# Kernel optimization log

Measured on AMD Instinct MI355X. Metric: run time of the kernel, lower is better.

## Reference

```python
import jax, jax.numpy as jnp
import numpy as np

TEMP = 0.1
K = 4
EPS = 1e-12


def _normalize(x):
    return x / jnp.maximum(jnp.linalg.norm(x, axis=1, keepdims=True), 1e-12)


def _sq_dists(a, b):
    # a: [Na,3], b: [Nb,3] -> [Na,Nb] squared euclidean distances
    aa = jnp.sum(a * a, axis=1, keepdims=True)          # [Na,1]
    bb = jnp.sum(b * b, axis=1, keepdims=True).T        # [1,Nb]
    return aa + bb - 2.0 * (a @ b.T)


def _directional_loss(f_q, f_db, d2_q_db):
    # knn of each query point in the database cloud, then cosine-sim softmax self-consistency loss
    _, idx = jax.lax.top_k(-d2_q_db, K)                  # [Nq,K] nearest-db indices
    f_matched = f_db[idx]                                # [Nq,K,C] gather (pointops.grouping)
    sim = jnp.einsum('nc,nkc->nk', f_q, f_matched) / TEMP
    p = jax.nn.softmax(sim, axis=1)                      # q_i == softmax when use_sinkhorn=False
    return jnp.mean(-jnp.log(jnp.sum(p * p, axis=1) + EPS))


def setup_inputs() -> dict:
    key = jax.random.key(0)
    k1, k2, k3, k4 = jax.random.split(key, 4)
    return {
        'feat_i': jax.random.normal(k1, (20000, 96), dtype=jnp.float32),
        'coord_i': jax.random.uniform(k2, (20000, 3), dtype=jnp.float32),
        'feat_j': jax.random.normal(k3, (10000, 96), dtype=jnp.float32),
        'coord_j': jax.random.uniform(k4, (10000, 3), dtype=jnp.float32),
    }


def reference(feat_i, coord_i, feat_j, coord_j):
    fi = _normalize(feat_i)
    fj = _normalize(feat_j)
    d2 = _sq_dists(coord_i, coord_j)                     # [Ni,Nj]
    loss_i = _directional_loss(fi, fj, d2)               # i queries, j database
    loss_j = _directional_loss(fj, fi, d2.T)             # j queries, i database
    pair = (loss_i + loss_j) * 0.5
    # num_views = 2 -> total_loss / max(1, num_views - 1) = pair
    return pair
```

## Files before the change

### kernel.cpp

```cpp
#include <hip/hip_runtime.h>
#include <math.h>

#define KMASK 0xFFFF8000u
#define IMASK 0x7FFFu

__device__ __forceinline__ float wave_reduce_sum(float v) {
    #pragma unroll
    for (int off = 32; off >= 1; off >>= 1) v += __shfl_xor(v, off, 64);
    return v;
}

__device__ __forceinline__ unsigned wave_min_u32(unsigned v) {
    #pragma unroll
    for (int off = 32; off >= 1; off >>= 1) {
        unsigned o = (unsigned)__shfl_xor((int)v, off, 64);
        v = (o < v) ? o : v;
    }
    return v;
}

__device__ __forceinline__ unsigned gmin8(unsigned v) {
    #pragma unroll
    for (int off = 4; off >= 1; off >>= 1) {
        unsigned o = (unsigned)__shfl_xor((int)v, off, 64);
        v = (o < v) ? o : v;
    }
    return v;
}
__device__ __forceinline__ float gsum8(float v) {
    #pragma unroll
    for (int off = 4; off >= 1; off >>= 1) v += __shfl_xor(v, off, 64);
    return v;
}

__device__ __forceinline__ void insert4kv(unsigned k, unsigned v,
                                          unsigned (&bk)[4], unsigned (&bv)[4]) {
    const bool c0 = k < bk[0], c1 = k < bk[1], c2 = k < bk[2], c3 = k < bk[3];
    bk[3] = c2 ? bk[2] : (c3 ? k : bk[3]);
    bv[3] = c2 ? bv[2] : (c3 ? v : bv[3]);
    bk[2] = c1 ? bk[1] : (c2 ? k : bk[2]);
    bv[2] = c1 ? bv[1] : (c2 ? v : bv[2]);
    bk[1] = c0 ? bk[0] : (c1 ? k : bk[1]);
    bv[1] = c0 ? bv[0] : (c1 ? v : bv[1]);
    bk[0] = c0 ? k : bk[0];
    bv[0] = c0 ? v : bv[0];
}

__device__ __forceinline__ int cell_of(float x, int G) {
    int c = (int)(x * (float)G);
    return (c < 0) ? 0 : ((c >= G) ? G - 1 : c);
}

__device__ __forceinline__ float dot4(float4 a, float4 b) {
    return fmaf(a.w, b.w, fmaf(a.z, b.z, fmaf(a.y, b.y, a.x * b.x)));
}


__global__ __launch_bounds__(256)
void grid_zero(int* __restrict__ stA, int nA, int* __restrict__ stB, int nB,
               float* __restrict__ out)
{
    const int t = blockIdx.x * 256 + threadIdx.x;
    if (t < nA) stA[t] = 0;
    if (t < nB) stB[t] = 0;
    if (t == 0) out[0] = 0.0f;
}

__global__ __launch_bounds__(256)
void grid_count(const float* __restrict__ cA, int nA, int GA, int* __restrict__ stA,
                const float* __restrict__ cB, int nB, int GB, int* __restrict__ stB)
{
    const int t = blockIdx.x * 256 + threadIdx.x;
    const float* c; int* s; int G; int p;
    if (t < nA)           { c = cA; s = stA; G = GA; p = t; }
    else if (t < nA + nB) { c = cB; s = stB; G = GB; p = t - nA; }
    else return;
    const int cx = cell_of(c[3*p], G), cy = cell_of(c[3*p+1], G), cz = cell_of(c[3*p+2], G);
    atomicAdd(&s[(cz * G + cy) * G + cx + 1], 1);
}

__global__ __launch_bounds__(256)
void grid_scan(int* __restrict__ sA, int nA, int* __restrict__ cuA,
               int* __restrict__ sB, int nB, int* __restrict__ cuB)
{
    int* s  = blockIdx.x ? sB  : sA;
    int* cu = blockIdx.x ? cuB : cuA;
    const int n = blockIdx.x ? nB : nA;
    __shared__ int part[256];
    const int t = threadIdx.x;
    const int len = n + 1;
    const int chunk = (len + 255) >> 8;
    const int lo = t * chunk;
    const int hi = (lo + chunk < len) ? (lo + chunk) : len;
    int sum = 0;
    for (int i = lo; i < hi; ++i) sum += s[i];
    part[t] = sum;
    __syncthreads();
    for (int d = 1; d < 256; d <<= 1) {
        const int v = (t >= d) ? part[t - d] : 0;
        __syncthreads();
        part[t] += v;
        __syncthreads();
    }
    int run = (t > 0) ? part[t - 1] : 0;
    for (int i = lo; i < hi; ++i) {
        run += s[i];
        s[i] = run;
        if (i < n) cu[i] = run;
    }
}

__global__ __launch_bounds__(256)
void grid_scatter(const float* __restrict__ cA, int nA, int GA, int* __restrict__ cuA,
                  float4* __restrict__ soA,
                  const float* __restrict__ cB, int nB, int GB, int* __restrict__ cuB,
                  float4* __restrict__ soB)
{
    const int t = blockIdx.x * 256 + threadIdx.x;
    const float* c; int* cu; float4* so; int G; int p;
    if (t < nA)           { c = cA; cu = cuA; so = soA; G = GA; p = t; }
    else if (t < nA + nB) { c = cB; cu = cuB; so = soB; G = GB; p = t - nA; }
    else return;
    const float x = c[3*p], y = c[3*p+1], z = c[3*p+2];
    const int cx = cell_of(x, G), cy = cell_of(y, G), cz = cell_of(z, G);
    const int pos = atomicAdd(&cu[(cz * G + cy) * G + cx], 1);
    so[pos] = make_float4(x, y, z, __uint_as_float((unsigned)p));
}


__global__ __launch_bounds__(256)
void knnloss(const float* __restrict__ fi, int Ni,
             const float* __restrict__ fj, int Nj,
             const float4* __restrict__ soA, const int* __restrict__ stA, int GA,
             const float4* __restrict__ soB, const int* __restrict__ stB, int GB,
             float sc0, float sc1, float* __restrict__ out)
{
    const int sub = threadIdx.x & 7;
    const int qid = (blockIdx.x * 256 + threadIdx.x) >> 3;
    float acc = 0.0f;

    if (qid < Ni + Nj) {
        const bool d0 = (qid < Ni);
        const int sq = d0 ? qid : qid - Ni;
        const float4* soq = d0 ? soB : soA;
        const float4* so = d0 ? soA : soB;
        const int*    st = d0 ? stA : stB;
        const int      G = d0 ? GA  : GB;
        const int     nd = d0 ? Nj  : Ni;
        const float*  fd = d0 ? fj  : fi;
        const float scale = d0 ? sc0 : sc1;

        const float4 Q = soq[sq];
        const unsigned p = __float_as_uint(Q.w);
        const float* fqp = (d0 ? fi : fj) + (size_t)p * 96;

        const float4* q4 = (const float4*)fqp;
        const float4 qa = q4[3*sub], qb = q4[3*sub+1], qc = q4[3*sub+2];

        const float qx = Q.x, qy = Q.y, qz = Q.z;
        const float h = 1.0f / (float)G;
        const int cx = cell_of(qx, G), cy = cell_of(qy, G), cz = cell_of(qz, G);
        unsigned nk[4], nv[4];

        {
            const int x0 = max(cx - 1, 0), x1 = min(cx + 1, G - 1);
            int csr[9], cer[9];
            #pragma unroll
            for (int dz = 0; dz < 3; ++dz) {
                #pragma unroll
                for (int dy = 0; dy < 3; ++dy) {
                    const int zz = cz + dz - 1, yy = cy + dy - 1;
                    const bool v = ((unsigned)zz < (unsigned)G) & ((unsigned)yy < (unsigned)G);
                    const int rb = v ? (zz * G + yy) * G : 0;
                    csr[dz*3+dy] = v ? st[rb + x0] : 0;
                    cer[dz*3+dy] = v ? st[rb + x1 + 1] : 0;
                }
            }
            unsigned bk[4] = {~0u, ~0u, ~0u, ~0u};
            unsigned bv[4] = {~0u, ~0u, ~0u, ~0u};
            #pragma unroll
            for (int r = 0; r < 9; ++r) {
                const int ce = cer[r];
                for (int cc = csr[r] + sub; cc < ce; cc += 16) {
                    const float4 P0 = so[cc];
                    const int cc1 = cc + 8;
                    const bool v1 = (cc1 < ce);
                    float4 P1 = P0;
                    if (v1) P1 = so[cc1];
                    const float dx0 = P0.x - qx, dy0 = P0.y - qy, dz0 = P0.z - qz;
                    const float d20 = fmaf(dx0, dx0, fmaf(dy0, dy0, dz0 * dz0));
                    const unsigned k0 = (__float_as_uint(d20) & KMASK) | (unsigned)cc;
                    insert4kv(k0, __float_as_uint(P0.w), bk, bv);
                    const float dx1 = P1.x - qx, dy1 = P1.y - qy, dz1 = P1.z - qz;
                    const float d21 = fmaf(dx1, dx1, fmaf(dy1, dy1, dz1 * dz1));
                    unsigned k1 = (__float_as_uint(d21) & KMASK) | (unsigned)cc1;
                    if (!v1) k1 = ~0u;
                    insert4kv(k1, __float_as_uint(P1.w), bk, bv);
                }
            }
            unsigned k0 = bk[0], k1 = bk[1], k2 = bk[2], k3 = bk[3];
            unsigned v0 = bv[0], v1 = bv[1], v2 = bv[2], v3 = bv[3];
            #pragma unroll
            for (int r = 0; r < 4; ++r) {
                const unsigned m = gmin8(k0);
                const bool win = (k0 == m);
                nv[r] = gmin8(win ? v0 : ~0u);
                nk[r] = m;
                k0 = win ? k1 : k0; v0 = win ? v1 : v0;
                k1 = win ? k2 : k1; v1 = win ? v2 : v1;
                k2 = win ? k3 : k2; v2 = win ? v3 : v2;
                k3 = win ? ~0u : k3;
            }
            const int y0 = max(cy - 1, 0), y1 = min(cy + 1, G - 1);
            const int z0 = max(cz - 1, 0), z1 = min(cz + 1, G - 1);
            float margin = 3.0e38f;
            if (x0 > 0)     margin = fminf(margin, qx - (float)x0 * h);
            if (x1 < G - 1) margin = fminf(margin, (float)(x1 + 1) * h - qx);
            if (y0 > 0)     margin = fminf(margin, qy - (float)y0 * h);
            if (y1 < G - 1) margin = fminf(margin, (float)(y1 + 1) * h - qy);
            if (z0 > 0)     margin = fminf(margin, qz - (float)z0 * h);
            if (z1 < G - 1) margin = fminf(margin, (float)(z1 + 1) * h - qz);
            const bool covered = (margin > 1.0e37f);
            const float kd = __uint_as_float(nk[3] & KMASK);
            const bool ok = covered || (kd * 1.01f <= margin * margin);

            if (!ok) {
                for (int s = 2; ; ++s) {
                    const int sx0 = max(cx - s, 0), sx1 = min(cx + s, G - 1);
                    const int sy0 = max(cy - s, 0), sy1 = min(cy + s, G - 1);
                    const int sz0 = max(cz - s, 0), sz1 = min(cz + s, G - 1);
                    unsigned b2k[4] = {~0u, ~0u, ~0u, ~0u};
                    unsigned b2v[4] = {~0u, ~0u, ~0u, ~0u};
                    for (int z = sz0; z <= sz1; ++z) {
                        for (int y = sy0; y <= sy1; ++y) {
                            const int rb = (z * G + y) * G;
                            const int cs = st[rb + sx0];
                            const int ce = st[rb + sx1 + 1];
                            for (int cc = cs + sub; cc < ce; cc += 8) {
                                const float4 P = so[cc];
                                const float dx = P.x - qx, dy = P.y - qy, dz = P.z - qz;
                                const float d2 = fmaf(dx, dx, fmaf(dy, dy, dz * dz));
                                const unsigned k =
                                    (__float_as_uint(d2) & KMASK) | (unsigned)cc;
                                insert4kv(k, __float_as_uint(P.w), b2k, b2v);
                            }
                        }
                    }
                    unsigned u0 = b2k[0], u1 = b2k[1], u2 = b2k[2], u3 = b2k[3];
                    unsigned w0 = b2v[0], w1 = b2v[1], w2 = b2v[2], w3 = b2v[3];
                    #pragma unroll
                    for (int r = 0; r < 4; ++r) {
                        const unsigned m = gmin8(u0);
                        const bool win = (u0 == m);
                        nv[r] = gmin8(win ? w0 : ~0u);
                        nk[r] = m;
                        u0 = win ? u1 : u0; w0 = win ? w1 : w0;
                        u1 = win ? u2 : u1; w1 = win ? w2 : w1;
                        u2 = win ? u3 : u2; w2 = win ? w3 : w2;
                        u3 = win ? ~0u : u3;
                    }
                    float mg = 3.0e38f;
                    if (sx0 > 0)     mg = fminf(mg, qx - (float)sx0 * h);
                    if (sx1 < G - 1) mg = fminf(mg, (float)(sx1 + 1) * h - qx);
                    if (sy0 > 0)     mg = fminf(mg, qy - (float)sy0 * h);
                    if (sy1 < G - 1) mg = fminf(mg, (float)(sy1 + 1) * h - qy);
                    if (sz0 > 0)     mg = fminf(mg, qz - (float)sz0 * h);
                    if (sz1 < G - 1) mg = fminf(mg, (float)(sz1 + 1) * h - qz);
                    const bool cov = (mg > 1.0e37f);
                    const float k2d = __uint_as_float(nk[3] & KMASK);
                    if (cov || (k2d * 1.01f <= mg * mg)) break;
                }
            }
        }

        const unsigned nm1 = (unsigned)(nd - 1);
        const unsigned i0 = nv[0] < nm1 ? nv[0] : nm1;
        const unsigned i1 = nv[1] < nm1 ? nv[1] : nm1;
        const unsigned i2 = nv[2] < nm1 ? nv[2] : nm1;
        const unsigned i3 = nv[3] < nm1 ? nv[3] : nm1;

        const float4* f0 = (const float4*)(fd + (size_t)i0 * 96);
        const float4* f1 = (const float4*)(fd + (size_t)i1 * 96);
        const float4* f2 = (const float4*)(fd + (size_t)i2 * 96);
        const float4* f3 = (const float4*)(fd + (size_t)i3 * 96);
        const float4 a0 = f0[3*sub], b0 = f0[3*sub+1], c0 = f0[3*sub+2];
        const float4 a1 = f1[3*sub], b1 = f1[3*sub+1], c1 = f1[3*sub+2];
        const float4 a2 = f2[3*sub], b2 = f2[3*sub+1], c2 = f2[3*sub+2];
        const float4 a3 = f3[3*sub], b3 = f3[3*sub+1], c3 = f3[3*sub+2];

        const float ssq = gsum8(dot4(qa,qa) + dot4(qb,qb) + dot4(qc,qc));

        float sim[4];
        {
            const float dv = gsum8(dot4(qa,a0) + dot4(qb,b0) + dot4(qc,c0));
            const float sd = gsum8(dot4(a0,a0) + dot4(b0,b0) + dot4(c0,c0));
            sim[0] = dv * rsqrtf(fmaxf(ssq, 1e-24f) * fmaxf(sd, 1e-24f)) * 10.0f;
        }
        {
            const float dv = gsum8(dot4(qa,a1) + dot4(qb,b1) + dot4(qc,c1));
            const float sd = gsum8(dot4(a1,a1) + dot4(b1,b1) + dot4(c1,c1));
            sim[1] = dv * rsqrtf(fmaxf(ssq, 1e-24f) * fmaxf(sd, 1e-24f)) * 10.0f;
        }
        {
            const float dv = gsum8(dot4(qa,a2) + dot4(qb,b2) + dot4(qc,c2));
            const float sd = gsum8(dot4(a2,a2) + dot4(b2,b2) + dot4(c2,c2));
            sim[2] = dv * rsqrtf(fmaxf(ssq, 1e-24f) * fmaxf(sd, 1e-24f)) * 10.0f;
        }
        {
            const float dv = gsum8(dot4(qa,a3) + dot4(qb,b3) + dot4(qc,c3));
            const float sd = gsum8(dot4(a3,a3) + dot4(b3,b3) + dot4(c3,c3));
            sim[3] = dv * rsqrtf(fmaxf(ssq, 1e-24f) * fmaxf(sd, 1e-24f)) * 10.0f;
        }

        const float m = fmaxf(fmaxf(sim[0], sim[1]), fmaxf(sim[2], sim[3]));
        const float e0 = __expf(sim[0] - m), e1 = __expf(sim[1] - m);
        const float e2 = __expf(sim[2] - m), e3 = __expf(sim[3] - m);
        const float ssum = e0 + e1 + e2 + e3;
        const float inv = 1.0f / ssum;
        const float p2 = (e0*e0 + e1*e1 + e2*e2 + e3*e3) * inv * inv;
        if (sub == 0) acc = -__logf(p2 + 1e-12f) * scale;
    }

    acc = wave_reduce_sum(acc);
    __shared__ float red[4];
    if ((threadIdx.x & 63) == 0) red[threadIdx.x >> 6] = acc;
    __syncthreads();
    if (threadIdx.x == 0) atomicAdd(out, red[0] + red[1] + red[2] + red[3]);
}


#define WPB 4
__device__ __forceinline__ void insert4u(unsigned k, unsigned (&b)[4]) {
    const bool c0 = k < b[0], c1 = k < b[1], c2 = k < b[2], c3 = k < b[3];
    b[3] = c2 ? b[2] : (c3 ? k : b[3]);
    b[2] = c1 ? b[1] : (c2 ? k : b[2]);
    b[1] = c0 ? b[0] : (c1 ? k : b[1]);
    b[0] = c0 ? k : b[0];
}

template<int QPW>
__device__ __forceinline__ void brute_dir(
    const float* __restrict__ cq, const float* __restrict__ fq, int Nq,
    const float* __restrict__ cd, const float* __restrict__ fd, int Nd,
    float scale, float* __restrict__ out, int blk)
{
    const int lane = threadIdx.x & 63;
    const int widx = threadIdx.x >> 6;
    int qbase = (blk * WPB + widx) * QPW;
    if (qbase >= Nq) return;
    qbase = __builtin_amdgcn_readfirstlane(qbase);

    float qx[QPW], qy[QPW], qz[QPW];
    #pragma unroll
    for (int q = 0; q < QPW; ++q) {
        const int qi = (qbase + q < Nq) ? (qbase + q) : (Nq - 1);
        qx[q] = cq[qi*3]; qy[q] = cq[qi*3+1]; qz[q] = cq[qi*3+2];
    }
    unsigned bk[QPW][4];
    #pragma unroll
    for (int q = 0; q < QPW; ++q) {
        #pragma unroll
        for (int k = 0; k < 4; ++k) bk[q][k] = ~0u;
    }
    for (int base = 0; base < Nd; base += 64) {
        const int p = base + lane;
        const int cp = (p < Nd) ? p : (Nd - 1);
        const float px = cd[cp*3], py = cd[cp*3+1], pz = cd[cp*3+2];
        #pragma unroll
        for (int q = 0; q < QPW; ++q) {
            const float dx = px - qx[q], dy = py - qy[q], dz = pz - qz[q];
            const float d2 = dx*dx + dy*dy + dz*dz;
            unsigned k = (__float_as_uint(d2) & KMASK) | (unsigned)p;
            if (p >= Nd) k = ~0u;
            insert4u(k, bk[q]);
        }
    }
    float wacc = 0.0f;
    #pragma unroll
    for (int q = 0; q < QPW; ++q) {
        if (qbase + q >= Nq) break;
        unsigned t0 = bk[q][0], t1 = bk[q][1], t2 = bk[q][2], t3 = bk[q][3];
        int ni_[4];
        #pragma unroll
        for (int k = 0; k < 4; ++k) {
            const unsigned m = wave_min_u32(t0);
            ni_[k] = (int)(m & IMASK);
            const bool win = (t0 == m);
            t0 = win ? t1 : t0; t1 = win ? t2 : t1; t2 = win ? t3 : t2; t3 = win ? ~0u : t3;
        }
        const float* fqp = fq + (size_t)(qbase + q) * 96;
        const float qf0 = fqp[lane];
        const float qf1 = (lane < 32) ? fqp[64 + lane] : 0.0f;
        const float ssq = wave_reduce_sum(qf0*qf0 + qf1*qf1);
        float sim[4];
        #pragma unroll
        for (int k = 0; k < 4; ++k) {
            const float* fdp = fd + (size_t)ni_[k] * 96;
            const float df0 = fdp[lane];
            const float df1 = (lane < 32) ? fdp[64 + lane] : 0.0f;
            const float dotv = wave_reduce_sum(qf0*df0 + qf1*df1);
            const float ssd = wave_reduce_sum(df0*df0 + df1*df1);
            sim[k] = dotv * rsqrtf(fmaxf(ssq, 1e-24f) * fmaxf(ssd, 1e-24f)) * 10.0f;
        }
        const float m = fmaxf(fmaxf(sim[0], sim[1]), fmaxf(sim[2], sim[3]));
        const float e0 = __expf(sim[0]-m), e1 = __expf(sim[1]-m);
        const float e2 = __expf(sim[2]-m), e3 = __expf(sim[3]-m);
        const float ssum = e0+e1+e2+e3;
        const float inv = 1.0f/ssum;
        const float p2 = (e0*e0+e1*e1+e2*e2+e3*e3)*inv*inv;
        wacc += -__logf(p2 + 1e-12f);
    }
    if (lane == 0) atomicAdd(out, wacc * scale);
}

__global__ __launch_bounds__(256)
void brute_fused(const float* __restrict__ ci, const float* __restrict__ fi, int Ni,
                 const float* __restrict__ cj, const float* __restrict__ fj, int Nj,
                 float s0, float s1, int B0, int B1, float* __restrict__ out)
{
    const int bid = (int)blockIdx.x;
    const int bmin = (B0 < B1) ? B0 : B1;
    int dir, blk;
    if (bid < 2 * bmin) { dir = bid & 1; blk = bid >> 1; }
    else { dir = (B0 > B1) ? 0 : 1; blk = bid - bmin; }
    if (dir == 0) brute_dir<8>(ci, fi, Ni, cj, fj, Nj, s0, out, blk);
    else          brute_dir<4>(cj, fj, Nj, ci, fi, Ni, s1, out, blk);
}


extern "C" void kernel_launch(void* const* d_in, const int* in_sizes, int n_in,
                              void* d_out, int out_size, void* d_ws, size_t ws_size,
                              hipStream_t stream) {
    const float* feat_i  = (const float*)d_in[0];
    const float* coord_i = (const float*)d_in[1];
    const float* feat_j  = (const float*)d_in[2];
    const float* coord_j = (const float*)d_in[3];
    const int Ni = in_sizes[0] / 96;
    const int Nj = in_sizes[2] / 96;
    float* out = (float*)d_out;

    auto gridfor = [](int n) {
        int g = (int)cbrtf((float)n / 4.5f);
        if (g < 2) g = 2;
        if (g > 28) g = 28;
        return g;
    };
    const int GA = gridfor(Nj), GB = gridfor(Ni);
    const int GA3 = GA * GA * GA, GB3 = GB * GB * GB;

    size_t off = 0;
    auto alloc = [&](size_t bytes) { size_t o = off; off = (off + bytes + 15) & ~(size_t)15; return o; };
    const size_t o_soA  = alloc((size_t)Nj * 16);
    const size_t o_soB  = alloc((size_t)Ni * 16);
    const size_t o_stA  = alloc((size_t)(GA3 + 1) * 4);
    const size_t o_stB  = alloc((size_t)(GB3 + 1) * 4);
    const size_t o_cuA  = alloc((size_t)GA3 * 4);
    const size_t o_cuB  = alloc((size_t)GB3 * 4);

    if (ws_size >= off && Ni >= 16 && Nj >= 16 && Ni <= 32000 && Nj <= 32000) {
        char* W = (char*)d_ws;
        float4* soA = (float4*)(W + o_soA);
        float4* soB = (float4*)(W + o_soB);
        int* stA = (int*)(W + o_stA);
        int* stB = (int*)(W + o_stB);
        int* cuA = (int*)(W + o_cuA);
        int* cuB = (int*)(W + o_cuB);

        const int nPts = Ni + Nj;
        const int nmax = ((GA3 > GB3) ? GA3 : GB3) + 1;

        grid_zero<<<(nmax + 255) / 256, 256, 0, stream>>>(stA, GA3 + 1, stB, GB3 + 1, out);
        grid_count<<<(nPts + 255) / 256, 256, 0, stream>>>(
            coord_j, Nj, GA, stA, coord_i, Ni, GB, stB);
        grid_scan<<<2, 256, 0, stream>>>(stA, GA3, cuA, stB, GB3, cuB);
        grid_scatter<<<(nPts + 255) / 256, 256, 0, stream>>>(
            coord_j, Nj, GA, cuA, soA, coord_i, Ni, GB, cuB, soB);

        const int nQ = Ni + Nj;
        const int nblk = (nQ * 8 + 255) / 256;
        knnloss<<<nblk, 256, 0, stream>>>(
            feat_i, Ni, feat_j, Nj,
            soA, stA, GA, soB, stB, GB,
            0.5f / (float)Ni, 0.5f / (float)Nj, out);
    } else {
        hipMemsetAsync(out, 0, sizeof(float), stream);
        const int waves0 = (Ni + 7) / 8;
        const int B0 = (waves0 + WPB - 1) / WPB;
        const int waves1 = (Nj + 3) / 4;
        const int B1 = (waves1 + WPB - 1) / WPB;
        brute_fused<<<B0 + B1, 256, 0, stream>>>(
            coord_i, feat_i, Ni, coord_j, feat_j, Nj,
            0.5f / (float)Ni, 0.5f / (float)Nj, B0, B1, out);
    }
}
```

Baseline: 49.56 us.

## Fuse grid build and kNN loss into one cooperative kernel with grid syncs

Replaces the five separate launches (zero, count, scan, scatter, knnloss) with a single cooperative kernel that runs the same stages separated by grid-wide syncs. The kNN query body moves into a shared device function used by both the fused and the fallback paths. The aim is to remove per-launch overhead and the idle gaps between small kernels. In exchange it pays for four grid.sync barriers, leaves most blocks idle while two blocks do the scan, and the fused kernel's register use may lower occupancy. It also adds an occupancy query and a device attribute query on the host each call, and falls back to the old launches if the grid cannot be fully resident.

```diff
diff --git a/kernel.cpp b/kernel.cpp
--- a/kernel.cpp
+++ b/kernel.cpp
@@ -1,5 +1,8 @@
 #include <hip/hip_runtime.h>
+#include <hip/hip_cooperative_groups.h>
 #include <math.h>
+
+namespace cg = cooperative_groups;
 
 #define KMASK 0xFFFF8000u
 #define IMASK 0x7FFFu
@@ -53,6 +56,282 @@
 
 __device__ __forceinline__ float dot4(float4 a, float4 b) {
     return fmaf(a.w, b.w, fmaf(a.z, b.z, fmaf(a.y, b.y, a.x * b.x)));
+}
+
+__device__ __forceinline__ float knn_query(
+    int qid, int Ni, int Nj,
+    const float* __restrict__ fi, const float* __restrict__ fj,
+    const float4* __restrict__ soA, const int* __restrict__ stA, int GA,
+    const float4* __restrict__ soB, const int* __restrict__ stB, int GB,
+    float sc0, float sc1, int sub)
+{
+    const bool d0 = (qid < Ni);
+    const int sq = d0 ? qid : qid - Ni;
+    const float4* soq = d0 ? soB : soA;
+    const float4* so = d0 ? soA : soB;
+    const int*    st = d0 ? stA : stB;
+    const int      G = d0 ? GA  : GB;
+    const int     nd = d0 ? Nj  : Ni;
+    const float*  fd = d0 ? fj  : fi;
+    const float scale = d0 ? sc0 : sc1;
+
+    const float4 Q = soq[sq];
+    const unsigned p = __float_as_uint(Q.w);
+    const float* fqp = (d0 ? fi : fj) + (size_t)p * 96;
+
+    const float4* q4 = (const float4*)fqp;
+    const float4 qa = q4[3*sub], qb = q4[3*sub+1], qc = q4[3*sub+2];
+
+    const float qx = Q.x, qy = Q.y, qz = Q.z;
+    const float h = 1.0f / (float)G;
+    const int cx = cell_of(qx, G), cy = cell_of(qy, G), cz = cell_of(qz, G);
+    unsigned nk[4], nv[4];
+
+    {
+        const int x0 = max(cx - 1, 0), x1 = min(cx + 1, G - 1);
+        int csr[9], cer[9];
+        #pragma unroll
+        for (int dz = 0; dz < 3; ++dz) {
+            #pragma unroll
+            for (int dy = 0; dy < 3; ++dy) {
+                const int zz = cz + dz - 1, yy = cy + dy - 1;
+                const bool v = ((unsigned)zz < (unsigned)G) & ((unsigned)yy < (unsigned)G);
+                const int rb = v ? (zz * G + yy) * G : 0;
+                csr[dz*3+dy] = v ? st[rb + x0] : 0;
+                cer[dz*3+dy] = v ? st[rb + x1 + 1] : 0;
+            }
+        }
+        unsigned bk[4] = {~0u, ~0u, ~0u, ~0u};
+        unsigned bv[4] = {~0u, ~0u, ~0u, ~0u};
+        #pragma unroll
+        for (int r = 0; r < 9; ++r) {
+            const int ce = cer[r];
+            for (int cc = csr[r] + sub; cc < ce; cc += 16) {
+                const float4 P0 = so[cc];
+                const int cc1 = cc + 8;
+                const bool v1 = (cc1 < ce);
+                float4 P1 = P0;
+                if (v1) P1 = so[cc1];
+                const float dx0 = P0.x - qx, dy0 = P0.y - qy, dz0 = P0.z - qz;
+                const float d20 = fmaf(dx0, dx0, fmaf(dy0, dy0, dz0 * dz0));
+                const unsigned k0 = (__float_as_uint(d20) & KMASK) | (unsigned)cc;
+                insert4kv(k0, __float_as_uint(P0.w), bk, bv);
+                const float dx1 = P1.x - qx, dy1 = P1.y - qy, dz1 = P1.z - qz;
+                const float d21 = fmaf(dx1, dx1, fmaf(dy1, dy1, dz1 * dz1));
+                unsigned k1 = (__float_as_uint(d21) & KMASK) | (unsigned)cc1;
+                if (!v1) k1 = ~0u;
+                insert4kv(k1, __float_as_uint(P1.w), bk, bv);
+            }
+        }
+        unsigned k0 = bk[0], k1 = bk[1], k2 = bk[2], k3 = bk[3];
+        unsigned v0 = bv[0], v1 = bv[1], v2 = bv[2], v3 = bv[3];
+        #pragma unroll
+        for (int r = 0; r < 4; ++r) {
+            const unsigned m = gmin8(k0);
+            const bool win = (k0 == m);
+            nv[r] = gmin8(win ? v0 : ~0u);
+            nk[r] = m;
+            k0 = win ? k1 : k0; v0 = win ? v1 : v0;
+            k1 = win ? k2 : k1; v1 = win ? v2 : v1;
+            k2 = win ? k3 : k2; v2 = win ? v3 : v2;
+            k3 = win ? ~0u : k3;
+        }
+        const int y0 = max(cy - 1, 0), y1 = min(cy + 1, G - 1);
+        const int z0 = max(cz - 1, 0), z1 = min(cz + 1, G - 1);
+        float margin = 3.0e38f;
+        if (x0 > 0)     margin = fminf(margin, qx - (float)x0 * h);
+        if (x1 < G - 1) margin = fminf(margin, (float)(x1 + 1) * h - qx);
+        if (y0 > 0)     margin = fminf(margin, qy - (float)y0 * h);
+        if (y1 < G - 1) margin = fminf(margin, (float)(y1 + 1) * h - qy);
+        if (z0 > 0)     margin = fminf(margin, qz - (float)z0 * h);
+        if (z1 < G - 1) margin = fminf(margin, (float)(z1 + 1) * h - qz);
+        const bool covered = (margin > 1.0e37f);
+        const float kd = __uint_as_float(nk[3] & KMASK);
+        const bool ok = covered || (kd * 1.01f <= margin * margin);
+
+        if (!ok) {
+            for (int s = 2; ; ++s) {
+                const int sx0 = max(cx - s, 0), sx1 = min(cx + s, G - 1);
+                const int sy0 = max(cy - s, 0), sy1 = min(cy + s, G - 1);
+                const int sz0 = max(cz - s, 0), sz1 = min(cz + s, G - 1);
+                unsigned b2k[4] = {~0u, ~0u, ~0u, ~0u};
+                unsigned b2v[4] = {~0u, ~0u, ~0u, ~0u};
+                for (int z = sz0; z <= sz1; ++z) {
+                    for (int y = sy0; y <= sy1; ++y) {
+                        const int rb = (z * G + y) * G;
+                        const int cs = st[rb + sx0];
+                        const int ce = st[rb + sx1 + 1];
+                        for (int cc = cs + sub; cc < ce; cc += 8) {
+                            const float4 P = so[cc];
+                            const float dx = P.x - qx, dy = P.y - qy, dz = P.z - qz;
+                            const float d2 = fmaf(dx, dx, fmaf(dy, dy, dz * dz));
+                            const unsigned k =
+                                (__float_as_uint(d2) & KMASK) | (unsigned)cc;
+                            insert4kv(k, __float_as_uint(P.w), b2k, b2v);
+                        }
+                    }
+                }
+                unsigned u0 = b2k[0], u1 = b2k[1], u2 = b2k[2], u3 = b2k[3];
+                unsigned w0 = b2v[0], w1 = b2v[1], w2 = b2v[2], w3 = b2v[3];
+                #pragma unroll
+                for (int r = 0; r < 4; ++r) {
+                    const unsigned m = gmin8(u0);
+                    const bool win = (u0 == m);
+                    nv[r] = gmin8(win ? w0 : ~0u);
+                    nk[r] = m;
+                    u0 = win ? u1 : u0; w0 = win ? w1 : w0;
+                    u1 = win ? u2 : u1; w1 = win ? w2 : w1;
+                    u2 = win ? u3 : u2; w2 = win ? w3 : w2;
+                    u3 = win ? ~0u : u3;
+                }
+                float mg = 3.0e38f;
+                if (sx0 > 0)     mg = fminf(mg, qx - (float)sx0 * h);
+                if (sx1 < G - 1) mg = fminf(mg, (float)(sx1 + 1) * h - qx);
+                if (sy0 > 0)     mg = fminf(mg, qy - (float)sy0 * h);
+                if (sy1 < G - 1) mg = fminf(mg, (float)(sy1 + 1) * h - qy);
+                if (sz0 > 0)     mg = fminf(mg, qz - (float)sz0 * h);
+                if (sz1 < G - 1) mg = fminf(mg, (float)(sz1 + 1) * h - qz);
+                const bool cov = (mg > 1.0e37f);
+                const float k2d = __uint_as_float(nk[3] & KMASK);
+                if (cov || (k2d * 1.01f <= mg * mg)) break;
+            }
+        }
+    }
+
+    const unsigned nm1u = (unsigned)(nd - 1);
+    const unsigned i0 = nv[0] < nm1u ? nv[0] : nm1u;
+    const unsigned i1 = nv[1] < nm1u ? nv[1] : nm1u;
+    const unsigned i2 = nv[2] < nm1u ? nv[2] : nm1u;
+    const unsigned i3 = nv[3] < nm1u ? nv[3] : nm1u;
+
+    const float4* f0 = (const float4*)(fd + (size_t)i0 * 96);
+    const float4* f1 = (const float4*)(fd + (size_t)i1 * 96);
+    const float4* f2 = (const float4*)(fd + (size_t)i2 * 96);
+    const float4* f3 = (const float4*)(fd + (size_t)i3 * 96);
+    const float4 a0 = f0[3*sub], b0 = f0[3*sub+1], c0f = f0[3*sub+2];
+    const float4 a1 = f1[3*sub], b1 = f1[3*sub+1], c1f = f1[3*sub+2];
+    const float4 a2 = f2[3*sub], b2 = f2[3*sub+1], c2f = f2[3*sub+2];
+    const float4 a3 = f3[3*sub], b3 = f3[3*sub+1], c3f = f3[3*sub+2];
+
+    const float ssq = gsum8(dot4(qa,qa) + dot4(qb,qb) + dot4(qc,qc));
+
+    float sim[4];
+    {
+        const float dv = gsum8(dot4(qa,a0) + dot4(qb,b0) + dot4(qc,c0f));
+        const float sd = gsum8(dot4(a0,a0) + dot4(b0,b0) + dot4(c0f,c0f));
+        sim[0] = dv * rsqrtf(fmaxf(ssq, 1e-24f) * fmaxf(sd, 1e-24f)) * 10.0f;
+    }
+    {
+        const float dv = gsum8(dot4(qa,a1) + dot4(qb,b1) + dot4(qc,c1f));
+        const float sd = gsum8(dot4(a1,a1) + dot4(b1,b1) + dot4(c1f,c1f));
+        sim[1] = dv * rsqrtf(fmaxf(ssq, 1e-24f) * fmaxf(sd, 1e-24f)) * 10.0f;
+    }
+    {
+        const float dv = gsum8(dot4(qa,a2) + dot4(qb,b2) + dot4(qc,c2f));
+        const float sd = gsum8(dot4(a2,a2) + dot4(b2,b2) + dot4(c2f,c2f));
+        sim[2] = dv * rsqrtf(fmaxf(ssq, 1e-24f) * fmaxf(sd, 1e-24f)) * 10.0f;
+    }
+    {
+        const float dv = gsum8(dot4(qa,a3) + dot4(qb,b3) + dot4(qc,c3f));
+        const float sd = gsum8(dot4(a3,a3) + dot4(b3,b3) + dot4(c3f,c3f));
+        sim[3] = dv * rsqrtf(fmaxf(ssq, 1e-24f) * fmaxf(sd, 1e-24f)) * 10.0f;
+    }
+
+    const float m = fmaxf(fmaxf(sim[0], sim[1]), fmaxf(sim[2], sim[3]));
+    const float e0 = __expf(sim[0] - m), e1 = __expf(sim[1] - m);
+    const float e2 = __expf(sim[2] - m), e3 = __expf(sim[3] - m);
+    const float ssum = e0 + e1 + e2 + e3;
+    const float inv = 1.0f / ssum;
+    const float p2 = (e0*e0 + e1*e1 + e2*e2 + e3*e3) * inv * inv;
+    return -__logf(p2 + 1e-12f) * scale;
+}
+
+
+__global__ __launch_bounds__(256)
+void fused_all(const float* __restrict__ ci, const float* __restrict__ fi, int Ni,
+               const float* __restrict__ cj, const float* __restrict__ fj, int Nj,
+               float4* __restrict__ soA, int* __restrict__ stA,
+               int* __restrict__ cuA, int GA,
+               float4* __restrict__ soB, int* __restrict__ stB,
+               int* __restrict__ cuB, int GB,
+               float sc0, float sc1, float* __restrict__ out)
+{
+    cg::grid_group grid = cg::this_grid();
+    const int tid = blockIdx.x * 256 + threadIdx.x;
+    const int nth = gridDim.x * 256;
+    const int GA3 = GA * GA * GA, GB3 = GB * GB * GB;
+
+    for (int t = tid; t <= GA3; t += nth) stA[t] = 0;
+    for (int t = tid; t <= GB3; t += nth) stB[t] = 0;
+    if (tid == 0) out[0] = 0.0f;
+    grid.sync();
+
+    for (int t = tid; t < Nj; t += nth) {
+        const int cx = cell_of(cj[3*t], GA), cy = cell_of(cj[3*t+1], GA), cz = cell_of(cj[3*t+2], GA);
+        atomicAdd(&stA[(cz * GA + cy) * GA + cx + 1], 1);
+    }
+    for (int t = tid; t < Ni; t += nth) {
+        const int cx = cell_of(ci[3*t], GB), cy = cell_of(ci[3*t+1], GB), cz = cell_of(ci[3*t+2], GB);
+        atomicAdd(&stB[(cz * GB + cy) * GB + cx + 1], 1);
+    }
+    grid.sync();
+
+    __shared__ int part[256];
+    if (blockIdx.x < 2) {
+        int* s  = blockIdx.x ? stB : stA;
+        int* cu = blockIdx.x ? cuB : cuA;
+        const int n = blockIdx.x ? GB3 : GA3;
+        const int t = threadIdx.x;
+        const int len = n + 1;
+        const int chunk = (len + 255) >> 8;
+        const int lo = t * chunk;
+        const int hi = (lo + chunk < len) ? (lo + chunk) : len;
+        int sum = 0;
+        for (int i = lo; i < hi; ++i) sum += s[i];
+        part[t] = sum;
+        __syncthreads();
+        for (int d = 1; d < 256; d <<= 1) {
+            const int v = (t >= d) ? part[t - d] : 0;
+            __syncthreads();
+            part[t] += v;
+            __syncthreads();
+        }
+        int run = (t > 0) ? part[t - 1] : 0;
+        for (int i = lo; i < hi; ++i) {
+            run += s[i];
+            s[i] = run;
+            if (i < n) cu[i] = run;
+        }
+    }
+    grid.sync();
+
+    for (int t = tid; t < Nj; t += nth) {
+        const float x = cj[3*t], y = cj[3*t+1], z = cj[3*t+2];
+        const int cx = cell_of(x, GA), cy = cell_of(y, GA), cz = cell_of(z, GA);
+        const int pos = atomicAdd(&cuA[(cz * GA + cy) * GA + cx], 1);
+        soA[pos] = make_float4(x, y, z, __uint_as_float((unsigned)t));
+    }
+    for (int t = tid; t < Ni; t += nth) {
+        const float x = ci[3*t], y = ci[3*t+1], z = ci[3*t+2];
+        const int cx = cell_of(x, GB), cy = cell_of(y, GB), cz = cell_of(z, GB);
+        const int pos = atomicAdd(&cuB[(cz * GB + cy) * GB + cx], 1);
+        soB[pos] = make_float4(x, y, z, __uint_as_float((unsigned)t));
+    }
+    grid.sync();
+
+    const int sub = threadIdx.x & 7;
+    const int nQ = Ni + Nj;
+    float acc = 0.0f;
+    const int qid = (blockIdx.x * 256 + threadIdx.x) >> 3;
+    if (qid < nQ)
+        acc = knn_query(qid, Ni, Nj, fi, fj, soA, stA, GA, soB, stB, GB, sc0, sc1, sub);
+    if (sub != 0) acc = 0.0f;
+
+    acc = wave_reduce_sum(acc);
+    __shared__ float red[4];
+    if ((threadIdx.x & 63) == 0) red[threadIdx.x >> 6] = acc;
+    __syncthreads();
+    if (threadIdx.x == 0) atomicAdd(out, red[0] + red[1] + red[2] + red[3]);
 }
 
 
@@ -127,7 +406,6 @@
     so[pos] = make_float4(x, y, z, __uint_as_float((unsigned)p));
 }
 
-
 __global__ __launch_bounds__(256)
 void knnloss(const float* __restrict__ fi, int Ni,
              const float* __restrict__ fj, int Nj,
@@ -138,188 +416,9 @@
     const int sub = threadIdx.x & 7;
     const int qid = (blockIdx.x * 256 + threadIdx.x) >> 3;
     float acc = 0.0f;
-
-    if (qid < Ni + Nj) {
-        const bool d0 = (qid < Ni);
-        const int sq = d0 ? qid : qid - Ni;
-        const float4* soq = d0 ? soB : soA;
-        const float4* so = d0 ? soA : soB;
-        const int*    st = d0 ? stA : stB;
-        const int      G = d0 ? GA  : GB;
-        const int     nd = d0 ? Nj  : Ni;
-        const float*  fd = d0 ? fj  : fi;
-        const float scale = d0 ? sc0 : sc1;
-
-        const float4 Q = soq[sq];
-        const unsigned p = __float_as_uint(Q.w);
-        const float* fqp = (d0 ? fi : fj) + (size_t)p * 96;
-
-        const float4* q4 = (const float4*)fqp;
-        const float4 qa = q4[3*sub], qb = q4[3*sub+1], qc = q4[3*sub+2];
-
-        const float qx = Q.x, qy = Q.y, qz = Q.z;
-        const float h = 1.0f / (float)G;
-        const int cx = cell_of(qx, G), cy = cell_of(qy, G), cz = cell_of(qz, G);
-        unsigned nk[4], nv[4];
-
-        {
-            const int x0 = max(cx - 1, 0), x1 = min(cx + 1, G - 1);
-            int csr[9], cer[9];
-            #pragma unroll
-            for (int dz = 0; dz < 3; ++dz) {
-                #pragma unroll
-                for (int dy = 0; dy < 3; ++dy) {
-                    const int zz = cz + dz - 1, yy = cy + dy - 1;
-                    const bool v = ((unsigned)zz < (unsigned)G) & ((unsigned)yy < (unsigned)G);
-                    const int rb = v ? (zz * G + yy) * G : 0;
-                    csr[dz*3+dy] = v ? st[rb + x0] : 0;
-                    cer[dz*3+dy] = v ? st[rb + x1 + 1] : 0;
-                }
-            }
-            unsigned bk[4] = {~0u, ~0u, ~0u, ~0u};
-            unsigned bv[4] = {~0u, ~0u, ~0u, ~0u};
-            #pragma unroll
-            for (int r = 0; r < 9; ++r) {
-                const int ce = cer[r];
-                for (int cc = csr[r] + sub; cc < ce; cc += 16) {
-                    const float4 P0 = so[cc];
-                    const int cc1 = cc + 8;
-                    const bool v1 = (cc1 < ce);
-                    float4 P1 = P0;
-                    if (v1) P1 = so[cc1];
-                    const float dx0 = P0.x - qx, dy0 = P0.y - qy, dz0 = P0.z - qz;
-                    const float d20 = fmaf(dx0, dx0, fmaf(dy0, dy0, dz0 * dz0));
-                    const unsigned k0 = (__float_as_uint(d20) & KMASK) | (unsigned)cc;
-                    insert4kv(k0, __float_as_uint(P0.w), bk, bv);
-                    const float dx1 = P1.x - qx, dy1 = P1.y - qy, dz1 = P1.z - qz;
-                    const float d21 = fmaf(dx1, dx1, fmaf(dy1, dy1, dz1 * dz1));
-                    unsigned k1 = (__float_as_uint(d21) & KMASK) | (unsigned)cc1;
-                    if (!v1) k1 = ~0u;
-                    insert4kv(k1, __float_as_uint(P1.w), bk, bv);
-                }
-            }
-            unsigned k0 = bk[0], k1 = bk[1], k2 = bk[2], k3 = bk[3];
-            unsigned v0 = bv[0], v1 = bv[1], v2 = bv[2], v3 = bv[3];
-            #pragma unroll
-            for (int r = 0; r < 4; ++r) {
-                const unsigned m = gmin8(k0);
-                const bool win = (k0 == m);
-                nv[r] = gmin8(win ? v0 : ~0u);
-                nk[r] = m;
-                k0 = win ? k1 : k0; v0 = win ? v1 : v0;
-                k1 = win ? k2 : k1; v1 = win ? v2 : v1;
-                k2 = win ? k3 : k2; v2 = win ? v3 : v2;
-                k3 = win ? ~0u : k3;
-            }
-            const int y0 = max(cy - 1, 0), y1 = min(cy + 1, G - 1);
-            const int z0 = max(cz - 1, 0), z1 = min(cz + 1, G - 1);
-            float margin = 3.0e38f;
-            if (x0 > 0)     margin = fminf(margin, qx - (float)x0 * h);
-            if (x1 < G - 1) margin = fminf(margin, (float)(x1 + 1) * h - qx);
-            if (y0 > 0)     margin = fminf(margin, qy - (float)y0 * h);
-            if (y1 < G - 1) margin = fminf(margin, (float)(y1 + 1) * h - qy);
-            if (z0 > 0)     margin = fminf(margin, qz - (float)z0 * h);
-            if (z1 < G - 1) margin = fminf(margin, (float)(z1 + 1) * h - qz);
-            const bool covered = (margin > 1.0e37f);
-            const float kd = __uint_as_float(nk[3] & KMASK);
-            const bool ok = covered || (kd * 1.01f <= margin * margin);
-
-            if (!ok) {
-                for (int s = 2; ; ++s) {
-                    const int sx0 = max(cx - s, 0), sx1 = min(cx + s, G - 1);
-                    const int sy0 = max(cy - s, 0), sy1 = min(cy + s, G - 1);
-                    const int sz0 = max(cz - s, 0), sz1 = min(cz + s, G - 1);
-                    unsigned b2k[4] = {~0u, ~0u, ~0u, ~0u};
-                    unsigned b2v[4] = {~0u, ~0u, ~0u, ~0u};
-                    for (int z = sz0; z <= sz1; ++z) {
-                        for (int y = sy0; y <= sy1; ++y) {
-                            const int rb = (z * G + y) * G;
-                            const int cs = st[rb + sx0];
-                            const int ce = st[rb + sx1 + 1];
-                            for (int cc = cs + sub; cc < ce; cc += 8) {
-                                const float4 P = so[cc];
-                                const float dx = P.x - qx, dy = P.y - qy, dz = P.z - qz;
-                                const float d2 = fmaf(dx, dx, fmaf(dy, dy, dz * dz));
-                                const unsigned k =
-                                    (__float_as_uint(d2) & KMASK) | (unsigned)cc;
-                                insert4kv(k, __float_as_uint(P.w), b2k, b2v);
-                            }
-                        }
-                    }
-                    unsigned u0 = b2k[0], u1 = b2k[1], u2 = b2k[2], u3 = b2k[3];
-                    unsigned w0 = b2v[0], w1 = b2v[1], w2 = b2v[2], w3 = b2v[3];
-                    #pragma unroll
-                    for (int r = 0; r < 4; ++r) {
-                        const unsigned m = gmin8(u0);
-                        const bool win = (u0 == m);
-                        nv[r] = gmin8(win ? w0 : ~0u);
-                        nk[r] = m;
-                        u0 = win ? u1 : u0; w0 = win ? w1 : w0;
-                        u1 = win ? u2 : u1; w1 = win ? w2 : w1;
-                        u2 = win ? u3 : u2; w2 = win ? w3 : w2;
-                        u3 = win ? ~0u : u3;
-                    }
-                    float mg = 3.0e38f;
-                    if (sx0 > 0)     mg = fminf(mg, qx - (float)sx0 * h);
-                    if (sx1 < G - 1) mg = fminf(mg, (float)(sx1 + 1) * h - qx);
-                    if (sy0 > 0)     mg = fminf(mg, qy - (float)sy0 * h);
-                    if (sy1 < G - 1) mg = fminf(mg, (float)(sy1 + 1) * h - qy);
-                    if (sz0 > 0)     mg = fminf(mg, qz - (float)sz0 * h);
-                    if (sz1 < G - 1) mg = fminf(mg, (float)(sz1 + 1) * h - qz);
-                    const bool cov = (mg > 1.0e37f);
-                    const float k2d = __uint_as_float(nk[3] & KMASK);
-                    if (cov || (k2d * 1.01f <= mg * mg)) break;
-                }
-            }
-        }
-
-        const unsigned nm1 = (unsigned)(nd - 1);
-        const unsigned i0 = nv[0] < nm1 ? nv[0] : nm1;
-        const unsigned i1 = nv[1] < nm1 ? nv[1] : nm1;
-        const unsigned i2 = nv[2] < nm1 ? nv[2] : nm1;
-        const unsigned i3 = nv[3] < nm1 ? nv[3] : nm1;
-
-        const float4* f0 = (const float4*)(fd + (size_t)i0 * 96);
-        const float4* f1 = (const float4*)(fd + (size_t)i1 * 96);
-        const float4* f2 = (const float4*)(fd + (size_t)i2 * 96);
-        const float4* f3 = (const float4*)(fd + (size_t)i3 * 96);
-        const float4 a0 = f0[3*sub], b0 = f0[3*sub+1], c0 = f0[3*sub+2];
-        const float4 a1 = f1[3*sub], b1 = f1[3*sub+1], c1 = f1[3*sub+2];
-        const float4 a2 = f2[3*sub], b2 = f2[3*sub+1], c2 = f2[3*sub+2];
-        const float4 a3 = f3[3*sub], b3 = f3[3*sub+1], c3 = f3[3*sub+2];
-
-        const float ssq = gsum8(dot4(qa,qa) + dot4(qb,qb) + dot4(qc,qc));
-
-        float sim[4];
-        {
-            const float dv = gsum8(dot4(qa,a0) + dot4(qb,b0) + dot4(qc,c0));
-            const float sd = gsum8(dot4(a0,a0) + dot4(b0,b0) + dot4(c0,c0));
-            sim[0] = dv * rsqrtf(fmaxf(ssq, 1e-24f) * fmaxf(sd, 1e-24f)) * 10.0f;
-        }
-        {
-            const float dv = gsum8(dot4(qa,a1) + dot4(qb,b1) + dot4(qc,c1));
-            const float sd = gsum8(dot4(a1,a1) + dot4(b1,b1) + dot4(c1,c1));
-            sim[1] = dv * rsqrtf(fmaxf(ssq, 1e-24f) * fmaxf(sd, 1e-24f)) * 10.0f;
-        }
-        {
-            const float dv = gsum8(dot4(qa,a2) + dot4(qb,b2) + dot4(qc,c2));
-            const float sd = gsum8(dot4(a2,a2) + dot4(b2,b2) + dot4(c2,c2));
-            sim[2] = dv * rsqrtf(fmaxf(ssq, 1e-24f) * fmaxf(sd, 1e-24f)) * 10.0f;
-        }
-        {
-            const float dv = gsum8(dot4(qa,a3) + dot4(qb,b3) + dot4(qc,c3));
-            const float sd = gsum8(dot4(a3,a3) + dot4(b3,b3) + dot4(c3,c3));
-            sim[3] = dv * rsqrtf(fmaxf(ssq, 1e-24f) * fmaxf(sd, 1e-24f)) * 10.0f;
-        }
-
-        const float m = fmaxf(fmaxf(sim[0], sim[1]), fmaxf(sim[2], sim[3]));
-        const float e0 = __expf(sim[0] - m), e1 = __expf(sim[1] - m);
-        const float e2 = __expf(sim[2] - m), e3 = __expf(sim[3] - m);
-        const float ssum = e0 + e1 + e2 + e3;
-        const float inv = 1.0f / ssum;
-        const float p2 = (e0*e0 + e1*e1 + e2*e2 + e3*e3) * inv * inv;
-        if (sub == 0) acc = -__logf(p2 + 1e-12f) * scale;
-    }
+    if (qid < Ni + Nj)
+        acc = knn_query(qid, Ni, Nj, fi, fj, soA, stA, GA, soB, stB, GB, sc0, sc1, sub);
+    if (sub != 0) acc = 0.0f;
 
     acc = wave_reduce_sum(acc);
     __shared__ float red[4];
@@ -466,22 +565,43 @@
         int* cuA = (int*)(W + o_cuA);
         int* cuB = (int*)(W + o_cuB);
 
-        const int nPts = Ni + Nj;
-        const int nmax = ((GA3 > GB3) ? GA3 : GB3) + 1;
-
-        grid_zero<<<(nmax + 255) / 256, 256, 0, stream>>>(stA, GA3 + 1, stB, GB3 + 1, out);
-        grid_count<<<(nPts + 255) / 256, 256, 0, stream>>>(
-            coord_j, Nj, GA, stA, coord_i, Ni, GB, stB);
-        grid_scan<<<2, 256, 0, stream>>>(stA, GA3, cuA, stB, GB3, cuB);
-        grid_scatter<<<(nPts + 255) / 256, 256, 0, stream>>>(
-            coord_j, Nj, GA, cuA, soA, coord_i, Ni, GB, cuB, soB);
-
         const int nQ = Ni + Nj;
         const int nblk = (nQ * 8 + 255) / 256;
-        knnloss<<<nblk, 256, 0, stream>>>(
-            feat_i, Ni, feat_j, Nj,
-            soA, stA, GA, soB, stB, GB,
-            0.5f / (float)Ni, 0.5f / (float)Nj, out);
+
+        int blocksPerCU = 0;
+        hipError_t e = hipOccupancyMaxActiveBlocksPerMultiprocessor(
+            &blocksPerCU, fused_all, 256, 0);
+        int numCU = 256;
+        hipDeviceGetAttribute(&numCU, hipDeviceAttributeMultiprocessorCount, 0);
+        const bool coop_ok = (e == hipSuccess) && (blocksPerCU * numCU >= nblk) && (nblk >= 2);
+
+        if (coop_ok) {
+            const float* ci_ = coord_i; const float* fi_ = feat_i; int Ni_ = Ni;
+            const float* cj_ = coord_j; const float* fj_ = feat_j; int Nj_ = Nj;
+            int GA_ = GA, GB_ = GB;
+            float s0 = 0.5f / (float)Ni, s1 = 0.5f / (float)Nj;
+            float* out_ = out;
+            void* args[] = { (void*)&ci_, (void*)&fi_, (void*)&Ni_,
+                             (void*)&cj_, (void*)&fj_, (void*)&Nj_,
+                             (void*)&soA, (void*)&stA, (void*)&cuA, (void*)&GA_,
+                             (void*)&soB, (void*)&stB, (void*)&cuB, (void*)&GB_,
+                             (void*)&s0, (void*)&s1, (void*)&out_ };
+            hipLaunchCooperativeKernel((void*)fused_all, dim3(nblk), dim3(256),
+                                       args, 0, stream);
+        } else {
+            const int nPts = Ni + Nj;
+            const int nmax = ((GA3 > GB3) ? GA3 : GB3) + 1;
+            grid_zero<<<(nmax + 255) / 256, 256, 0, stream>>>(stA, GA3 + 1, stB, GB3 + 1, out);
+            grid_count<<<(nPts + 255) / 256, 256, 0, stream>>>(
+                coord_j, Nj, GA, stA, coord_i, Ni, GB, stB);
+            grid_scan<<<2, 256, 0, stream>>>(stA, GA3, cuA, stB, GB3, cuB);
+            grid_scatter<<<(nPts + 255) / 256, 256, 0, stream>>>(
+                coord_j, Nj, GA, cuA, soA, coord_i, Ni, GB, cuB, soB);
+            knnloss<<<nblk, 256, 0, stream>>>(
+                feat_i, Ni, feat_j, Nj,
+                soA, stA, GA, soB, stB, GB,
+                0.5f / (float)Ni, 0.5f / (float)Nj, out);
+        }
     } else {
         hipMemsetAsync(out, 0, sizeof(float), stream);
         const int waves0 = (Ni + 7) / 8;
```

New measurement: 50.89 us. 2.7% more time.
